# Performance work log

Measured on AMD Instinct MI355X. Metric: run time of the kernel, lower is better.

Reference implementation:

```python
import jax, jax.numpy as jnp
import numpy as np

TAU = 2.0
VTH = 0.7
VRESET = 0.0
ALPHA = 4.0
MAX_ITER = 10
WARM = 2
T, B, F = 1024, 32, 512


def setup_inputs() -> dict:
    key = jax.random.key(0)
    x = jax.random.normal(key, (T, B, F), dtype=jnp.float32)
    v_init = jnp.zeros((B, F), dtype=jnp.float32)
    return {"x": x, "v_init": v_init}


def _shift(y, y_init):
    # [y_init, y[0], ..., y[T-2]]
    return jnp.concatenate([y_init[None], y[:-1]], axis=0)


def _solve_linear_recurrence(a, b, y0):
    # y[t] = a[t] * y[t-1] + b[t], y[-1] = y0; parallel via associative scan
    def comb(l, r):
        al, bl = l
        ar, br = r
        return ar * al, ar * bl + br
    A, Bc = jax.lax.associative_scan(comb, (a, b))
    return A * y0[None] + Bc


def _warmstart(x, v_init):
    # first K steps of the continuous (no-reset) dynamics, rest zeros
    K = min(WARM, x.shape[0])
    v = v_init
    rows = []
    for t in range(K):  # K=2, tiny fixed unroll
        h = v + (x[t] - v) / TAU
        rows.append(h)
        v = h
    guess = jnp.zeros_like(x)
    return guess.at[:K].set(jnp.stack(rows, axis=0))


def _forward(x, v_init):
    y = _warmstart(x, v_init)
    decay = 1.0 - 1.0 / TAU
    for _ in range(MAX_ITER):  # fixed iteration count (check_convergence=False)
        ys = _shift(y, v_init)            # (T,B,F)
        h = ys + (x - ys) / TAU           # L[y]: continuous dynamics, no reset
        hc = jnp.clip(h, -20.0, 20.0)
        s = jax.nn.sigmoid(ALPHA * (hc - VTH))
        sg = ALPHA * s * (1.0 - s)        # surrogate gradient
        G = -(decay * (1.0 - sg * (1.0 - VRESET)))  # diagonal Jacobian (T,B,F)
        rhs = h + G * ys
        y = _solve_linear_recurrence(-G, rhs, v_init)
    spike = (y >= VTH).astype(y.dtype)
    return spike, y


def reference(x, v_init):
    return _forward(x, v_init)
```

## Files before the change

### kernel.cpp

```cpp
#include <hip/hip_runtime.h>

#pragma clang fp contract(off)

namespace {
constexpr int T_ = 1024;
constexpr int B_ = 32;
constexpr int F_ = 512;
constexpr int BF_ = B_ * F_;
constexpr long TBF_ = (long)T_ * BF_;
constexpr int NITER = 10;
constexpr int NTHR = 256;

typedef float v2f __attribute__((ext_vector_type(2)));

constexpr float KLOG = 5.770780163555852f;
constexpr float CLOG = 4.0395461144890964f;

__device__ __forceinline__ int swz(int bb) { return bb ^ ((bb >> 3) & 7); }

struct ABp { v2f A, B; };
__device__ __forceinline__ ABp combp(ABp l, ABp r) {
  ABp o;
  o.A = r.A * l.A;
  o.B = __builtin_elementwise_fma(r.A, l.B, r.B);
  return o;
}

template <int CTRL, int RM>
__device__ __forceinline__ float dppf(float oldv, float src) {
  return __builtin_bit_cast(
      float, __builtin_amdgcn_update_dpp(__builtin_bit_cast(int, oldv),
                                         __builtin_bit_cast(int, src), CTRL,
                                         RM, 0xf, false));
}

template <int CTRL, int RM>
__device__ __forceinline__ ABp scan_step(ABp S) {
  ABp P;
  P.A.x = dppf<CTRL, RM>(1.0f, S.A.x);
  P.A.y = dppf<CTRL, RM>(1.0f, S.A.y);
  P.B.x = dppf<CTRL, RM>(0.0f, S.B.x);
  P.B.y = dppf<CTRL, RM>(0.0f, S.B.y);
  return combp(P, S);
}
}

__global__ __launch_bounds__(NTHR, 3) void deer_lif_kernel(
    const float* __restrict__ x, const float* __restrict__ v_init,
    float* __restrict__ out) {
  __shared__ float smem[8192];

  const int raw = blockIdx.x;
  const int blk = (raw & 7) * 256 + (raw >> 3);

  const int b  = blk >> 6;
  const int f0 = (blk & 63) << 3;

  const int tid = threadIdx.x;
  const int rt = tid >> 1;
  const int c0 = (tid & 1) << 2;
  const int wr0 = c0 >> 1;

  const float* xb = x + (long)b * F_ + f0 + c0;
#pragma unroll
  for (int p = 0; p < 8; ++p) {
    const int t = rt + (p << 7);
    const float4 v = *reinterpret_cast<const float4*>(xb + (long)t * BF_);
    const int base = (swz(t >> 1) << 2) + ((t & 1) << 1);
    float2 lo, hi;
    lo.x = v.x; lo.y = v.y;
    hi.x = v.z; hi.y = v.w;
    *reinterpret_cast<float2*>(&smem[wr0 * 2048 + base]) = lo;
    *reinterpret_cast<float2*>(&smem[(wr0 + 1) * 2048 + base]) = hi;
  }
  __syncthreads();

  const int w = tid >> 6;
  const int lane = tid & 63;
  const bool lz = (lane == 0);

  v2f v0;
  v0.x = v_init[b * F_ + f0 + 2 * w];
  v0.y = v_init[b * F_ + f0 + 2 * w + 1];

  v2f xp[16];
#pragma unroll
  for (int q = 0; q < 8; ++q) {
    const int bbs = swz((lane << 3) + q);
    const float4 v =
        *reinterpret_cast<const float4*>(&smem[w * 2048 + (bbs << 2)]);
    xp[2 * q].x = v.x;
    xp[2 * q].y = v.y;
    xp[2 * q + 1].x = v.z;
    xp[2 * q + 1].y = v.w;
  }

  v2f y[16];
#pragma unroll
  for (int j = 0; j < 16; ++j) y[j] = (v2f){0.0f, 0.0f};
  if (lz) {
    const v2f h0 = v0 + (xp[0] - v0) * 0.5f;
    const v2f h1 = h0 + (xp[1] - h0) * 0.5f;
    y[0] = h0;
    y[1] = h1;
  }

  const v2f half2 = {0.5f, 0.5f};
  const v2f one2 = {1.0f, 1.0f};
  const v2f nk2 = {-KLOG, -KLOG};
  const v2f ck2 = {CLOG, CLOG};
  const v2f lo2 = {-20.0f, -20.0f};

#pragma unroll 1
  for (int it = 0; it < NITER; ++it) {
    v2f ys0;
    ys0.x = dppf<0x138, 0xf>(v0.x, y[15].x);
    ys0.y = dppf<0x138, 0xf>(v0.y, y[15].y);

    v2f a[16], r[16];
    v2f cA, cB;
#pragma unroll
    for (int j = 0; j < 16; ++j) {
      const v2f ys = (j == 0) ? ys0 : y[j - 1];
      const v2f d = xp[j] - ys;
      const v2f h = __builtin_elementwise_fma(d, half2, ys);
      const v2f hc = __builtin_elementwise_max(h, lo2);
      const v2f z = __builtin_elementwise_fma(hc, nk2, ck2);
      v2f e;
      e.x = __builtin_amdgcn_exp2f(z.x);
      e.y = __builtin_amdgcn_exp2f(z.y);
      const v2f num = one2 - e;
      const v2f den = one2 + e;
      v2f rc;
      rc.x = __builtin_amdgcn_rcpf(den.x);
      rc.y = __builtin_amdgcn_rcpf(den.y);
      const v2f t = num * rc;
      const v2f t2 = t * t;
      const v2f aj = t2 * half2;
      const v2f rj = __builtin_elementwise_fma(-aj, ys, h);
      a[j] = aj;
      r[j] = rj;
      if (j == 0) {
        cA = aj;
        cB = rj;
      } else {
        cA = cA * aj;
        cB = __builtin_elementwise_fma(cB, aj, rj);
      }
    }

    ABp S;
    S.A = cA;
    S.B = cB;
    S = scan_step<0x111, 0xf>(S);
    S = scan_step<0x112, 0xf>(S);
    S = scan_step<0x114, 0xf>(S);
    S = scan_step<0x118, 0xf>(S);
    S = scan_step<0x142, 0xa>(S);
    S = scan_step<0x143, 0xc>(S);

    const v2f cinc = __builtin_elementwise_fma(S.A, v0, S.B);
    v2f carry;
    carry.x = dppf<0x138, 0xf>(v0.x, cinc.x);
    carry.y = dppf<0x138, 0xf>(v0.y, cinc.y);

#pragma unroll
    for (int j = 0; j < 16; ++j) {
      carry = __builtin_elementwise_fma(a[j], carry, r[j]);
      y[j] = carry;
    }
  }

#pragma unroll
  for (int q = 0; q < 8; ++q) {
    const int bbs = swz((lane << 3) + q);
    float4 v;
    v.x = y[2 * q].x;
    v.y = y[2 * q].y;
    v.z = y[2 * q + 1].x;
    v.w = y[2 * q + 1].y;
    *reinterpret_cast<float4*>(&smem[w * 2048 + (bbs << 2)]) = v;
  }
  __syncthreads();

  float* outs = out;
  float* outy = out + TBF_;
  const long cb = (long)b * F_ + f0 + c0;
#pragma unroll
  for (int p = 0; p < 8; ++p) {
    const int t = rt + (p << 7);
    const int base = (swz(t >> 1) << 2) + ((t & 1) << 1);
    const float2 lo = *reinterpret_cast<const float2*>(&smem[wr0 * 2048 + base]);
    const float2 hi =
        *reinterpret_cast<const float2*>(&smem[(wr0 + 1) * 2048 + base]);
    const float4 yv = make_float4(lo.x, lo.y, hi.x, hi.y);
    const float4 sv = make_float4(yv.x >= 0.7f ? 1.0f : 0.0f,
                                  yv.y >= 0.7f ? 1.0f : 0.0f,
                                  yv.z >= 0.7f ? 1.0f : 0.0f,
                                  yv.w >= 0.7f ? 1.0f : 0.0f);
    const long off = (long)t * BF_ + cb;
    *reinterpret_cast<float4*>(outy + off) = yv;
    *reinterpret_cast<float4*>(outs + off) = sv;
  }
}

extern "C" void kernel_launch(void* const* d_in, const int* in_sizes, int n_in,
                              void* d_out, int out_size, void* d_ws, size_t ws_size,
                              hipStream_t stream) {
  const float* x = (const float*)d_in[0];
  const float* v_init = (const float*)d_in[1];
  float* out = (float*)d_out;
  deer_lif_kernel<<<dim3(2048), dim3(NTHR), 0, stream>>>(x, v_init, out);
}
```

Baseline: 74.54 us.

## Halve LDS staging, raise occupancy, simplify sigmoid math, split serial chunk scans

The shared-memory staging buffer is halved, so x is loaded and y is written back in two 512-timestep phases with extra barriers, and the launch bound goes from 3 to 4 blocks per CU. The surrogate Jacobian is now computed as 0.5 - 2·s(1-s) directly from the sigmoid instead of through a tanh-squared form. The serial 16-step in-thread combine and carry propagation are split into four independent 4-step chains to shorten dependency latency. In exchange there are more barriers and some redundant LDS traffic, and register pressure under the tighter launch bound may cause spills.

```diff
diff --git a/kernel.cpp b/kernel.cpp
--- a/kernel.cpp
+++ b/kernel.cpp
@@ -3,11 +3,10 @@
 #pragma clang fp contract(off)
 
 namespace {
-constexpr int T_ = 1024;
 constexpr int B_ = 32;
 constexpr int F_ = 512;
 constexpr int BF_ = B_ * F_;
-constexpr long TBF_ = (long)T_ * BF_;
+constexpr long TBF_ = 16777216;
 constexpr int NITER = 10;
 constexpr int NTHR = 256;
 
@@ -43,12 +42,16 @@
   P.B.y = dppf<CTRL, RM>(0.0f, S.B.y);
   return combp(P, S);
 }
-}
-
-__global__ __launch_bounds__(NTHR, 3) void deer_lif_kernel(
+
+__device__ __forceinline__ v2f pkfma(v2f a, v2f b, v2f c) {
+  return __builtin_elementwise_fma(a, b, c);
+}
+}
+
+__global__ __launch_bounds__(NTHR, 4) void deer_lif_kernel(
     const float* __restrict__ x, const float* __restrict__ v_init,
     float* __restrict__ out) {
-  __shared__ float smem[8192];
+  __shared__ float smem[4096];
 
   const int raw = blockIdx.x;
   const int blk = (raw & 7) * 256 + (raw >> 3);
@@ -57,43 +60,53 @@
   const int f0 = (blk & 63) << 3;
 
   const int tid = threadIdx.x;
-  const int rt = tid >> 1;
   const int c0 = (tid & 1) << 2;
   const int wr0 = c0 >> 1;
 
-  const float* xb = x + (long)b * F_ + f0 + c0;
-#pragma unroll
-  for (int p = 0; p < 8; ++p) {
-    const int t = rt + (p << 7);
-    const float4 v = *reinterpret_cast<const float4*>(xb + (long)t * BF_);
-    const int base = (swz(t >> 1) << 2) + ((t & 1) << 1);
-    float2 lo, hi;
-    lo.x = v.x; lo.y = v.y;
-    hi.x = v.z; hi.y = v.w;
-    *reinterpret_cast<float2*>(&smem[wr0 * 2048 + base]) = lo;
-    *reinterpret_cast<float2*>(&smem[(wr0 + 1) * 2048 + base]) = hi;
-  }
-  __syncthreads();
-
   const int w = tid >> 6;
   const int lane = tid & 63;
+  const int ll = lane & 31;
+  const bool hihalf = (lane >= 32);
   const bool lz = (lane == 0);
 
-  v2f v0;
-  v0.x = v_init[b * F_ + f0 + 2 * w];
-  v0.y = v_init[b * F_ + f0 + 2 * w + 1];
+  const float* xb = x + (long)b * F_ + f0 + c0;
 
   v2f xp[16];
 #pragma unroll
-  for (int q = 0; q < 8; ++q) {
-    const int bbs = swz((lane << 3) + q);
-    const float4 v =
-        *reinterpret_cast<const float4*>(&smem[w * 2048 + (bbs << 2)]);
-    xp[2 * q].x = v.x;
-    xp[2 * q].y = v.y;
-    xp[2 * q + 1].x = v.z;
-    xp[2 * q + 1].y = v.w;
-  }
+  for (int p = 0; p < 2; ++p) {
+    if (p) __syncthreads();
+#pragma unroll
+    for (int k = 0; k < 4; ++k) {
+      const int lr = (tid >> 1) + (k << 7);
+      const int t = (p << 9) + lr;
+      const float4 v = *reinterpret_cast<const float4*>(xb + (long)t * BF_);
+      const int base = (swz(lr >> 1) << 2) + ((lr & 1) << 1);
+      *reinterpret_cast<float2*>(&smem[wr0 * 1024 + base]) =
+          make_float2(v.x, v.y);
+      *reinterpret_cast<float2*>(&smem[(wr0 + 1) * 1024 + base]) =
+          make_float2(v.z, v.w);
+    }
+    __syncthreads();
+#pragma unroll
+    for (int q = 0; q < 8; ++q) {
+      const int bbs = swz((ll << 3) + q);
+      const float4 v =
+          *reinterpret_cast<const float4*>(&smem[w * 1024 + (bbs << 2)]);
+      const v2f lo = {v.x, v.y};
+      const v2f hi = {v.z, v.w};
+      if (p == 0) {
+        xp[2 * q] = lo;
+        xp[2 * q + 1] = hi;
+      } else {
+        xp[2 * q] = hihalf ? lo : xp[2 * q];
+        xp[2 * q + 1] = hihalf ? hi : xp[2 * q + 1];
+      }
+    }
+  }
+
+  const float2 vi =
+      *reinterpret_cast<const float2*>(&v_init[b * F_ + f0 + 2 * w]);
+  v2f v0 = {vi.x, vi.y};
 
   v2f y[16];
 #pragma unroll
@@ -110,6 +123,7 @@
   const v2f nk2 = {-KLOG, -KLOG};
   const v2f ck2 = {CLOG, CLOG};
   const v2f lo2 = {-20.0f, -20.0f};
+  const v2f m22 = {-2.0f, -2.0f};
 
 #pragma unroll 1
   for (int it = 0; it < NITER; ++it) {
@@ -118,40 +132,45 @@
     ys0.y = dppf<0x138, 0xf>(v0.y, y[15].y);
 
     v2f a[16], r[16];
-    v2f cA, cB;
 #pragma unroll
     for (int j = 0; j < 16; ++j) {
       const v2f ys = (j == 0) ? ys0 : y[j - 1];
       const v2f d = xp[j] - ys;
-      const v2f h = __builtin_elementwise_fma(d, half2, ys);
+      const v2f h = pkfma(d, half2, ys);
       const v2f hc = __builtin_elementwise_max(h, lo2);
-      const v2f z = __builtin_elementwise_fma(hc, nk2, ck2);
+      const v2f z = pkfma(hc, nk2, ck2);
       v2f e;
       e.x = __builtin_amdgcn_exp2f(z.x);
       e.y = __builtin_amdgcn_exp2f(z.y);
-      const v2f num = one2 - e;
       const v2f den = one2 + e;
-      v2f rc;
-      rc.x = __builtin_amdgcn_rcpf(den.x);
-      rc.y = __builtin_amdgcn_rcpf(den.y);
-      const v2f t = num * rc;
-      const v2f t2 = t * t;
-      const v2f aj = t2 * half2;
-      const v2f rj = __builtin_elementwise_fma(-aj, ys, h);
+      v2f s;
+      s.x = __builtin_amdgcn_rcpf(den.x);
+      s.y = __builtin_amdgcn_rcpf(den.y);
+      const v2f oms = one2 - s;
+      const v2f pp = s * oms;
+      const v2f aj = pkfma(pp, m22, half2);
+      const v2f rj = pkfma(-aj, ys, h);
       a[j] = aj;
       r[j] = rj;
-      if (j == 0) {
-        cA = aj;
-        cB = rj;
-      } else {
-        cA = cA * aj;
-        cB = __builtin_elementwise_fma(cB, aj, rj);
-      }
-    }
-
+    }
+
+    v2f qA0 = a[0], qB0 = r[0];
+    v2f qA1 = a[4], qB1 = r[4];
+    v2f qA2 = a[8], qB2 = r[8];
+    v2f qA3 = a[12], qB3 = r[12];
+#pragma unroll
+    for (int k = 1; k < 4; ++k) {
+      qA0 = qA0 * a[k];      qB0 = pkfma(qB0, a[k], r[k]);
+      qA1 = qA1 * a[4 + k];  qB1 = pkfma(qB1, a[4 + k], r[4 + k]);
+      qA2 = qA2 * a[8 + k];  qB2 = pkfma(qB2, a[8 + k], r[8 + k]);
+      qA3 = qA3 * a[12 + k]; qB3 = pkfma(qB3, a[12 + k], r[12 + k]);
+    }
+    const v2f c01A = qA0 * qA1, c01B = pkfma(qB0, qA1, qB1);
+    const v2f c012A = c01A * qA2, c012B = pkfma(c01B, qA2, qB2);
     ABp S;
-    S.A = cA;
-    S.B = cB;
+    S.A = c012A * qA3;
+    S.B = pkfma(c012B, qA3, qB3);
+
     S = scan_step<0x111, 0xf>(S);
     S = scan_step<0x112, 0xf>(S);
     S = scan_step<0x114, 0xf>(S);
@@ -159,48 +178,60 @@
     S = scan_step<0x142, 0xa>(S);
     S = scan_step<0x143, 0xc>(S);
 
-    const v2f cinc = __builtin_elementwise_fma(S.A, v0, S.B);
-    v2f carry;
-    carry.x = dppf<0x138, 0xf>(v0.x, cinc.x);
-    carry.y = dppf<0x138, 0xf>(v0.y, cinc.y);
-
-#pragma unroll
-    for (int j = 0; j < 16; ++j) {
-      carry = __builtin_elementwise_fma(a[j], carry, r[j]);
-      y[j] = carry;
-    }
-  }
-
-#pragma unroll
-  for (int q = 0; q < 8; ++q) {
-    const int bbs = swz((lane << 3) + q);
-    float4 v;
-    v.x = y[2 * q].x;
-    v.y = y[2 * q].y;
-    v.z = y[2 * q + 1].x;
-    v.w = y[2 * q + 1].y;
-    *reinterpret_cast<float4*>(&smem[w * 2048 + (bbs << 2)]) = v;
-  }
-  __syncthreads();
+    const v2f cinc = pkfma(S.A, v0, S.B);
+    v2f cin;
+    cin.x = dppf<0x138, 0xf>(v0.x, cinc.x);
+    cin.y = dppf<0x138, 0xf>(v0.y, cinc.y);
+
+    v2f t0 = cin;
+    v2f t1 = pkfma(qA0, cin, qB0);
+    v2f t2 = pkfma(c01A, cin, c01B);
+    v2f t3 = pkfma(c012A, cin, c012B);
+#pragma unroll
+    for (int k = 0; k < 4; ++k) {
+      t0 = pkfma(a[k], t0, r[k]);           y[k] = t0;
+      t1 = pkfma(a[4 + k], t1, r[4 + k]);   y[4 + k] = t1;
+      t2 = pkfma(a[8 + k], t2, r[8 + k]);   y[8 + k] = t2;
+      t3 = pkfma(a[12 + k], t3, r[12 + k]); y[12 + k] = t3;
+    }
+  }
 
   float* outs = out;
   float* outy = out + TBF_;
   const long cb = (long)b * F_ + f0 + c0;
 #pragma unroll
-  for (int p = 0; p < 8; ++p) {
-    const int t = rt + (p << 7);
-    const int base = (swz(t >> 1) << 2) + ((t & 1) << 1);
-    const float2 lo = *reinterpret_cast<const float2*>(&smem[wr0 * 2048 + base]);
-    const float2 hi =
-        *reinterpret_cast<const float2*>(&smem[(wr0 + 1) * 2048 + base]);
-    const float4 yv = make_float4(lo.x, lo.y, hi.x, hi.y);
-    const float4 sv = make_float4(yv.x >= 0.7f ? 1.0f : 0.0f,
-                                  yv.y >= 0.7f ? 1.0f : 0.0f,
-                                  yv.z >= 0.7f ? 1.0f : 0.0f,
-                                  yv.w >= 0.7f ? 1.0f : 0.0f);
-    const long off = (long)t * BF_ + cb;
-    *reinterpret_cast<float4*>(outy + off) = yv;
-    *reinterpret_cast<float4*>(outs + off) = sv;
+  for (int p = 0; p < 2; ++p) {
+    __syncthreads();
+    if ((lane >> 5) == p) {
+#pragma unroll
+      for (int q = 0; q < 8; ++q) {
+        const int bbs = swz((ll << 3) + q);
+        float4 v;
+        v.x = y[2 * q].x;
+        v.y = y[2 * q].y;
+        v.z = y[2 * q + 1].x;
+        v.w = y[2 * q + 1].y;
+        *reinterpret_cast<float4*>(&smem[w * 1024 + (bbs << 2)]) = v;
+      }
+    }
+    __syncthreads();
+#pragma unroll
+    for (int k = 0; k < 4; ++k) {
+      const int lr = (tid >> 1) + (k << 7);
+      const int t = (p << 9) + lr;
+      const int base = (swz(lr >> 1) << 2) + ((lr & 1) << 1);
+      const float2 lo = *reinterpret_cast<const float2*>(&smem[wr0 * 1024 + base]);
+      const float2 h2 =
+          *reinterpret_cast<const float2*>(&smem[(wr0 + 1) * 1024 + base]);
+      const float4 yv = make_float4(lo.x, lo.y, h2.x, h2.y);
+      const float4 sv = make_float4(yv.x >= 0.7f ? 1.0f : 0.0f,
+                                    yv.y >= 0.7f ? 1.0f : 0.0f,
+                                    yv.z >= 0.7f ? 1.0f : 0.0f,
+                                    yv.w >= 0.7f ? 1.0f : 0.0f);
+      const long off = (long)t * BF_ + cb;
+      *reinterpret_cast<float4*>(outy + off) = yv;
+      *reinterpret_cast<float4*>(outs + off) = sv;
+    }
   }
 }
 
```

Result: slower. 76.54 us (+2.7%).
